# Kernel optimization log

Hardware: AMD Instinct MI355X
Metric: run time of the kernel (lower is better)

## Reference

```python
import jax, jax.numpy as jnp
import numpy as np

B, S, D = 8, 1024, 1024
H, DH = 16, 64  # num_attention_heads, attention_head_size; H*DH == D


def setup_inputs() -> dict:
    key = jax.random.key(0)
    ks = jax.random.split(key, 6)
    scale = 0.02
    return {
        "hidden_states": jax.random.normal(ks[0], (B, S, D), jnp.float32),
        "right_hidden_states": jax.random.normal(ks[1], (B, S, D), jnp.float32),
        "attention_mask": jnp.ones((B, S, S), jnp.float32),
        "Wq": jax.random.normal(ks[2], (D, H * DH), jnp.float32) * scale,
        "bq": jnp.zeros((H * DH,), jnp.float32),
        "Wk": jax.random.normal(ks[3], (D, H * DH), jnp.float32) * scale,
        "bk": jnp.zeros((H * DH,), jnp.float32),
        "Wv": jax.random.normal(ks[4], (D, H * DH), jnp.float32) * scale,
        "bv": jnp.zeros((H * DH,), jnp.float32),
    }


def _split_heads(x, b):
    # (B, S, H*DH) -> (B, H, S, DH)
    return x.reshape(b, -1, H, DH).transpose(0, 2, 1, 3)


def reference(hidden_states, right_hidden_states, attention_mask, Wq, bq, Wk, bk, Wv, bv):
    b = hidden_states.shape[0]
    q = _split_heads(hidden_states @ Wq + bq, b)          # (B,H,Sq,DH)
    k = _split_heads(right_hidden_states @ Wk + bk, b)    # (B,H,Sk,DH)
    v = _split_heads(right_hidden_states @ Wv + bv, b)    # (B,H,Sk,DH)

    scores = jnp.einsum("bhqd,bhkd->bhqk", q, k) / jnp.sqrt(jnp.asarray(DH, q.dtype))
    scores = jnp.sum(scores, axis=1, keepdims=True)       # (B,1,Sq,Sk) head-summed

    ext = (1.0 - attention_mask[:, None, :, :].astype(scores.dtype)) * -1e9
    probs = jax.nn.softmax(scores + ext, axis=-1)         # (B,1,Sq,Sk)

    ctx = jnp.matmul(probs, v)                            # broadcast -> (B,H,Sq,DH)
    # Faithful to original: reshape WITHOUT transposing heads back.
    return ctx.reshape(b, -1, H * DH)                     # (B,Sq,H*DH)
```

## Files before the change

kernel.cpp:

```cpp
#include <hip/hip_runtime.h>
#include <stdint.h>

constexpr int S = 1024;
constexpr int D = 1024;
constexpr int NB = 8;

typedef __bf16 bf16x8 __attribute__((ext_vector_type(8)));
typedef float floatx4 __attribute__((ext_vector_type(4)));

#define AS1 __attribute__((address_space(1)))
#define AS3 __attribute__((address_space(3)))

__device__ __forceinline__ unsigned short f2bf(float f) {
  unsigned u = __builtin_bit_cast(unsigned, f);
  u += 0x7fffu + ((u >> 16) & 1u);
  return (unsigned short)(u >> 16);
}

__device__ __forceinline__ void gload16(const void* g, void* l) {
  __builtin_amdgcn_global_load_lds((const AS1 unsigned int*)g, (AS3 unsigned int*)l, 16, 0, 0);
}

__global__ __launch_bounds__(256) void prep_kernel(const float4* __restrict__ hs4,
                                                   const float4* __restrict__ rhs4,
                                                   ushort4* __restrict__ hsb4,
                                                   ushort4* __restrict__ rhsb4, int n4,
                                                   const float* __restrict__ Wq,
                                                   const float* __restrict__ Wk,
                                                   const float* __restrict__ Wv,
                                                   unsigned short* __restrict__ Wcat) {
  __shared__ float tile[32][33];
  const int bid = blockIdx.x;
  if (bid < 16384) {
    int i = bid * 256 + threadIdx.x;
    const float4* src;
    ushort4* dst;
    int j;
    if (i < n4) {
      src = hs4; dst = hsb4; j = i;
    } else {
      src = rhs4; dst = rhsb4; j = i - n4;
    }
    float4 v = src[j];
    ushort4 o;
    o.x = f2bf(v.x); o.y = f2bf(v.y); o.z = f2bf(v.z); o.w = f2bf(v.w);
    dst[j] = o;
  } else {
    const int t = bid - 16384;
    const int z = t >> 10;
    const int r = t & 1023;
    const float* W = (z == 0) ? Wq : (z == 1) ? Wk : Wv;
    unsigned short* Wt = Wcat + (long long)z * D * D;
    const int bx = (r & 31) * 32;
    const int by = (r >> 5) * 32;
    const int x = threadIdx.x & 31;
    const int y0 = threadIdx.x >> 5;
    for (int i = 0; i < 4; ++i) {
      int y = y0 + i * 8;
      tile[y][x] = W[(by + y) * D + bx + x];
    }
    __syncthreads();
    for (int i = 0; i < 4; ++i) {
      int y = y0 + i * 8;
      Wt[(long long)(bx + y) * D + by + x] = f2bf(tile[x][y]);
    }
  }
}


#define GEMM_STAGE_SETUP(Abase, lda_, Bbase, ldb_)                            \
  const int srow = tid >> 2;                                                  \
  const int scg = (((tid & 3) ^ ((srow >> 1) & 3)) * 8);                      \
  const unsigned short* aG0 = (Abase) + (long long)srow * (lda_) + scg;       \
  const unsigned short* aG1 = aG0 + (long long)64 * (lda_);                   \
  const unsigned short* bG0 = (Bbase) + (long long)srow * (ldb_) + scg;       \
  const unsigned short* bG1 = bG0 + (long long)64 * (ldb_);                   \
  unsigned short* aL0 = As + w * 512;                                         \
  unsigned short* aL1 = As + w * 512 + 2048;                                  \
  unsigned short* bL0 = Bs + w * 512;                                         \
  unsigned short* bL1 = Bs + w * 512 + 2048;

#define GEMM_KLOOP(Klen)                                                               \
  for (int k0 = 0; k0 < (Klen); k0 += 32) {                                            \
    gload16(aG0 + k0, aL0);                                                            \
    gload16(aG1 + k0, aL1);                                                            \
    gload16(bG0 + k0, bL0);                                                            \
    gload16(bG1 + k0, bL1);                                                            \
    __syncthreads();                                                                   \
    bf16x8 af[4], bfr[4];                                                              \
    for (int t = 0; t < 4; ++t) {                                                      \
      af[t] = *reinterpret_cast<const bf16x8*>(As + (wm + t * 16 + r15) * 32 + pq);    \
      bfr[t] = *reinterpret_cast<const bf16x8*>(Bs + (wn + t * 16 + r15) * 32 + pq);   \
    }                                                                                  \
    for (int mt = 0; mt < 4; ++mt)                                                     \
      for (int nt = 0; nt < 4; ++nt)                                                   \
        acc[mt][nt] =                                                                  \
            __builtin_amdgcn_mfma_f32_16x16x32_bf16(af[mt], bfr[nt], acc[mt][nt], 0, 0, 0); \
    __syncthreads();                                                                   \
  }

#define GEMM_COMMON_IDX                  \
  const int tid = threadIdx.x;           \
  const int lane = tid & 63;             \
  const int w = tid >> 6;                \
  const int r15 = lane & 15;             \
  const int quad = lane >> 4;            \
  const int pq = (quad ^ ((r15 >> 1) & 3)) * 8; \
  const int wm = (w >> 1) * 64;          \
  const int wn = (w & 1) * 64;

#define GEMM_ACC_INIT                    \
  floatx4 acc[4][4];                     \
  for (int i = 0; i < 4; ++i)            \
    for (int j = 0; j < 4; ++j) acc[i][j] = {0.f, 0.f, 0.f, 0.f};

__global__ __launch_bounds__(256) void gemm_qkv_kernel(
    const unsigned short* __restrict__ hsb, const unsigned short* __restrict__ rhsb,
    const unsigned short* __restrict__ Wcat, unsigned short* __restrict__ Qm,
    unsigned short* __restrict__ Km, unsigned short* __restrict__ Vmt,
    const float* __restrict__ bq, const float* __restrict__ bk, const float* __restrict__ bv) {
  __shared__ __align__(16) unsigned short As[128 * 32];
  __shared__ __align__(16) unsigned short Bs[128 * 32];
  GEMM_COMMON_IDX
  const long long n0g = (long long)blockIdx.x * 128;
  const int seg = (int)(n0g >> 10);
  const long long m0 = (long long)blockIdx.y * 128;
  const unsigned short* A = ((seg == 0) ? hsb : rhsb) + m0 * D;
  const unsigned short* Bt = Wcat + n0g * D;
  const float* bias = (seg == 0) ? bq : (seg == 1) ? bk : bv;

  GEMM_STAGE_SETUP(A, D, Bt, D)
  GEMM_ACC_INIT
  GEMM_KLOOP(D)

  const long long nloc0 = n0g & 1023;
  for (int mt = 0; mt < 4; ++mt) {
    for (int nt = 0; nt < 4; ++nt) {
      const long long mrow = m0 + wm + mt * 16 + quad * 4;
      const long long nc = nloc0 + wn + nt * 16 + r15;
      const float bval = bias[nc];
      floatx4 v = acc[mt][nt];
      for (int e = 0; e < 4; ++e) {
        float val = v[e] + bval;
        long long m = mrow + e;
        if (seg == 0) {
          Qm[m * D + nc] = f2bf(val);
        } else if (seg == 1) {
          Km[m * D + nc] = f2bf(val);
        } else {
          Vmt[(m >> 10) * (long long)(S * D) + nc * S + (m & 1023)] = f2bf(val);
        }
      }
    }
  }
}

__global__ __launch_bounds__(256) void gemm_scores_kernel(
    const unsigned short* __restrict__ Qm, const unsigned short* __restrict__ Km,
    const float* __restrict__ mask, unsigned short* __restrict__ E,
    float* __restrict__ rowsumP) {
  __shared__ __align__(16) unsigned short As[128 * 32];
  __shared__ __align__(16) unsigned short Bs[128 * 32];
  GEMM_COMMON_IDX
  const int z = blockIdx.z;
  const long long m0 = (long long)blockIdx.y * 128;
  const long long n0 = (long long)blockIdx.x * 128;
  const unsigned short* A = Qm + (long long)z * S * D + m0 * D;
  const unsigned short* Bt = Km + (long long)z * S * D + n0 * D;

  GEMM_STAGE_SETUP(A, D, Bt, D)
  GEMM_ACC_INIT
  GEMM_KLOOP(D)

  const long long zE = (long long)z * S * 1024;
  float rowpart[4][4];
  for (int mt = 0; mt < 4; ++mt)
    for (int e = 0; e < 4; ++e) rowpart[mt][e] = 0.f;

  for (int mt = 0; mt < 4; ++mt) {
    for (int nt = 0; nt < 4; ++nt) {
      const long long mrow = m0 + wm + mt * 16 + quad * 4;
      const long long nc = n0 + wn + nt * 16 + r15;
      floatx4 v = acc[mt][nt];
      for (int e = 0; e < 4; ++e) {
        long long m = mrow + e;
        float mval = mask[zE + m * 1024 + nc];
        float sc = v[e] * 0.125f + (1.0f - mval) * -1e9f;
        float Ev = __expf(sc);
        E[zE + m * 1024 + nc] = f2bf(Ev);
        rowpart[mt][e] += Ev;
      }
    }
  }
  const int slot = ((int)blockIdx.x << 11) + ((wn >> 6) << 10);
  for (int mt = 0; mt < 4; ++mt) {
    for (int e = 0; e < 4; ++e) {
      float s = rowpart[mt][e];
      s += __shfl_xor(s, 1, 64);
      s += __shfl_xor(s, 2, 64);
      s += __shfl_xor(s, 4, 64);
      s += __shfl_xor(s, 8, 64);
      if (r15 == 0) {
        int mloc = (int)(m0 + wm + mt * 16 + quad * 4 + e);
        rowsumP[(z << 14) + slot + mloc] = s;
      }
    }
  }
}

__global__ __launch_bounds__(256) void gemm_ctx_kernel(const unsigned short* __restrict__ E,
                                                       const unsigned short* __restrict__ Vmt,
                                                       const float* __restrict__ rowsumP,
                                                       float* __restrict__ out) {
  __shared__ __align__(16) unsigned short As[128 * 32];
  __shared__ __align__(16) unsigned short Bs[128 * 32];
  __shared__ float rsinv[128];
  GEMM_COMMON_IDX
  const int z = blockIdx.z;
  const long long m0 = (long long)blockIdx.y * 128;
  const long long n0 = (long long)blockIdx.x * 128;
  const unsigned short* A = E + (long long)z * S * 1024 + m0 * 1024;
  const unsigned short* Bt = Vmt + (long long)z * S * D + n0 * D;

  if (tid < 128) {
    float s = 0.f;
    for (int t = 0; t < 16; ++t) s += rowsumP[(z << 14) + (t << 10) + (int)m0 + tid];
    rsinv[tid] = 1.0f / s;
  }

  GEMM_STAGE_SETUP(A, 1024, Bt, D)
  GEMM_ACC_INIT
  GEMM_KLOOP(1024)

  for (int mt = 0; mt < 4; ++mt) {
    for (int nt = 0; nt < 4; ++nt) {
      const int r0 = wm + mt * 16 + quad * 4;
      const long long ncol = n0 + wn + nt * 16 + r15;
      floatx4 v = acc[mt][nt];
      for (int e = 0; e < 4; ++e) {
        long long m = m0 + r0 + e;
        float val = v[e] * rsinv[r0 + e];
        out[(long long)z * S * D + (ncol >> 6) * (long long)(S * 64) + m * 64 + (ncol & 63)] =
            val;
      }
    }
  }
}

extern "C" void kernel_launch(void* const* d_in, const int* in_sizes, int n_in, void* d_out,
                              int out_size, void* d_ws, size_t ws_size, hipStream_t stream) {
  const float* hs = (const float*)d_in[0];
  const float* rhs = (const float*)d_in[1];
  const float* mask = (const float*)d_in[2];
  const float* Wq = (const float*)d_in[3];
  const float* bq = (const float*)d_in[4];
  const float* Wk = (const float*)d_in[5];
  const float* bk = (const float*)d_in[6];
  const float* Wv = (const float*)d_in[7];
  const float* bv = (const float*)d_in[8];
  float* out = (float*)d_out;
  char* ws = (char*)d_ws;
  const size_t MB = 1ull << 20;
  unsigned short* Wcat = (unsigned short*)(ws + 0 * MB);
  unsigned short* hsb = (unsigned short*)(ws + 6 * MB);
  unsigned short* rhsb = (unsigned short*)(ws + 22 * MB);
  unsigned short* Qm = (unsigned short*)(ws + 38 * MB);
  unsigned short* Km = (unsigned short*)(ws + 54 * MB);
  unsigned short* Vmt = (unsigned short*)(ws + 70 * MB);
  unsigned short* E = (unsigned short*)(ws + 6 * MB);
  float* rowsumP = (float*)(ws + 22 * MB);

  const int n4 = NB * S * D / 4;
  prep_kernel<<<16384 + 3072, 256, 0, stream>>>((const float4*)hs, (const float4*)rhs,
                                                (ushort4*)hsb, (ushort4*)rhsb, n4, Wq, Wk, Wv,
                                                Wcat);

  gemm_qkv_kernel<<<dim3(24, 64), 256, 0, stream>>>(hsb, rhsb, Wcat, Qm, Km, Vmt, bq, bk, bv);

  gemm_scores_kernel<<<dim3(8, 8, NB), 256, 0, stream>>>(Qm, Km, mask, E, rowsumP);

  gemm_ctx_kernel<<<dim3(8, 8, NB), 256, 0, stream>>>(E, Vmt, rowsumP, out);
}
```

Measured before the change: 299.4 us.

## Double-buffer LDS tiles in GEMM k-loop to overlap global loads with MFMA

```diff
diff --git a/kernel.cpp b/kernel.cpp
--- a/kernel.cpp
+++ b/kernel.cpp
@@ -74,29 +74,40 @@
   const unsigned short* aG0 = (Abase) + (long long)srow * (lda_) + scg;       \
   const unsigned short* aG1 = aG0 + (long long)64 * (lda_);                   \
   const unsigned short* bG0 = (Bbase) + (long long)srow * (ldb_) + scg;       \
-  const unsigned short* bG1 = bG0 + (long long)64 * (ldb_);                   \
-  unsigned short* aL0 = As + w * 512;                                         \
-  unsigned short* aL1 = As + w * 512 + 2048;                                  \
-  unsigned short* bL0 = Bs + w * 512;                                         \
-  unsigned short* bL1 = Bs + w * 512 + 2048;
-
-#define GEMM_KLOOP(Klen)                                                               \
-  for (int k0 = 0; k0 < (Klen); k0 += 32) {                                            \
-    gload16(aG0 + k0, aL0);                                                            \
-    gload16(aG1 + k0, aL1);                                                            \
-    gload16(bG0 + k0, bL0);                                                            \
-    gload16(bG1 + k0, bL1);                                                            \
-    __syncthreads();                                                                   \
-    bf16x8 af[4], bfr[4];                                                              \
-    for (int t = 0; t < 4; ++t) {                                                      \
-      af[t] = *reinterpret_cast<const bf16x8*>(As + (wm + t * 16 + r15) * 32 + pq);    \
-      bfr[t] = *reinterpret_cast<const bf16x8*>(Bs + (wn + t * 16 + r15) * 32 + pq);   \
-    }                                                                                  \
-    for (int mt = 0; mt < 4; ++mt)                                                     \
-      for (int nt = 0; nt < 4; ++nt)                                                   \
-        acc[mt][nt] =                                                                  \
-            __builtin_amdgcn_mfma_f32_16x16x32_bf16(af[mt], bfr[nt], acc[mt][nt], 0, 0, 0); \
-    __syncthreads();                                                                   \
+  const unsigned short* bG1 = bG0 + (long long)64 * (ldb_);
+
+#define GEMM_STAGE(bsel, ko)                      \
+  gload16(aG0 + (ko), As[bsel] + w * 512);        \
+  gload16(aG1 + (ko), As[bsel] + w * 512 + 2048); \
+  gload16(bG0 + (ko), Bs[bsel] + w * 512);        \
+  gload16(bG1 + (ko), Bs[bsel] + w * 512 + 2048);
+
+#define GEMM_KLOOP(Klen)                                                                 \
+  GEMM_STAGE(0, 0)                                                                       \
+  {                                                                                      \
+    const int NT_ = (Klen) / 32;                                                         \
+    for (int kt = 0; kt < NT_; ++kt) {                                                   \
+      const int cb = kt & 1;                                                             \
+      const int kn = (kt + 1 < NT_) ? (kt + 1) * 32 : kt * 32;                           \
+      GEMM_STAGE(cb ^ 1, kn)                                                             \
+      asm volatile("s_waitcnt vmcnt(4)" ::: "memory");                                   \
+      __builtin_amdgcn_s_barrier();                                                      \
+      asm volatile("" ::: "memory");                                                     \
+      const unsigned short* Acur = As[cb];                                               \
+      const unsigned short* Bcur = Bs[cb];                                               \
+      bf16x8 af[4], bfr[4];                                                              \
+      for (int t = 0; t < 4; ++t) {                                                      \
+        af[t] = *reinterpret_cast<const bf16x8*>(Acur + (wm + t * 16 + r15) * 32 + pq);  \
+        bfr[t] = *reinterpret_cast<const bf16x8*>(Bcur + (wn + t * 16 + r15) * 32 + pq); \
+      }                                                                                  \
+      for (int mt = 0; mt < 4; ++mt)                                                     \
+        for (int nt = 0; nt < 4; ++nt)                                                   \
+          acc[mt][nt] =                                                                  \
+              __builtin_amdgcn_mfma_f32_16x16x32_bf16(af[mt], bfr[nt], acc[mt][nt], 0, 0, 0); \
+      asm volatile("" ::: "memory");                                                     \
+      __builtin_amdgcn_s_barrier();                                                      \
+      asm volatile("" ::: "memory");                                                     \
+    }                                                                                    \
   }
 
 #define GEMM_COMMON_IDX                  \
@@ -119,8 +130,8 @@
     const unsigned short* __restrict__ Wcat, unsigned short* __restrict__ Qm,
     unsigned short* __restrict__ Km, unsigned short* __restrict__ Vmt,
     const float* __restrict__ bq, const float* __restrict__ bk, const float* __restrict__ bv) {
-  __shared__ __align__(16) unsigned short As[128 * 32];
-  __shared__ __align__(16) unsigned short Bs[128 * 32];
+  __shared__ __align__(16) unsigned short As[2][128 * 32];
+  __shared__ __align__(16) unsigned short Bs[2][128 * 32];
   GEMM_COMMON_IDX
   const long long n0g = (long long)blockIdx.x * 128;
   const int seg = (int)(n0g >> 10);
@@ -159,8 +170,8 @@
     const unsigned short* __restrict__ Qm, const unsigned short* __restrict__ Km,
     const float* __restrict__ mask, unsigned short* __restrict__ E,
     float* __restrict__ rowsumP) {
-  __shared__ __align__(16) unsigned short As[128 * 32];
-  __shared__ __align__(16) unsigned short Bs[128 * 32];
+  __shared__ __align__(16) unsigned short As[2][128 * 32];
+  __shared__ __align__(16) unsigned short Bs[2][128 * 32];
   GEMM_COMMON_IDX
   const int z = blockIdx.z;
   const long long m0 = (long long)blockIdx.y * 128;
@@ -212,8 +223,8 @@
                                                        const unsigned short* __restrict__ Vmt,
                                                        const float* __restrict__ rowsumP,
                                                        float* __restrict__ out) {
-  __shared__ __align__(16) unsigned short As[128 * 32];
-  __shared__ __align__(16) unsigned short Bs[128 * 32];
+  __shared__ __align__(16) unsigned short As[2][128 * 32];
+  __shared__ __align__(16) unsigned short Bs[2][128 * 32];
   __shared__ float rsinv[128];
   GEMM_COMMON_IDX
   const int z = blockIdx.z;
```

Result: slower. 319.8 us (+6.8%).

## Use K=64 per sync step and remap block indices for XCD locality

Applied to the files above, without the earlier changes.

```diff
diff --git a/kernel.cpp b/kernel.cpp
--- a/kernel.cpp
+++ b/kernel.cpp
@@ -74,29 +74,31 @@
   const unsigned short* aG0 = (Abase) + (long long)srow * (lda_) + scg;       \
   const unsigned short* aG1 = aG0 + (long long)64 * (lda_);                   \
   const unsigned short* bG0 = (Bbase) + (long long)srow * (ldb_) + scg;       \
-  const unsigned short* bG1 = bG0 + (long long)64 * (ldb_);                   \
-  unsigned short* aL0 = As + w * 512;                                         \
-  unsigned short* aL1 = As + w * 512 + 2048;                                  \
-  unsigned short* bL0 = Bs + w * 512;                                         \
-  unsigned short* bL1 = Bs + w * 512 + 2048;
-
-#define GEMM_KLOOP(Klen)                                                               \
-  for (int k0 = 0; k0 < (Klen); k0 += 32) {                                            \
-    gload16(aG0 + k0, aL0);                                                            \
-    gload16(aG1 + k0, aL1);                                                            \
-    gload16(bG0 + k0, bL0);                                                            \
-    gload16(bG1 + k0, bL1);                                                            \
-    __syncthreads();                                                                   \
-    bf16x8 af[4], bfr[4];                                                              \
-    for (int t = 0; t < 4; ++t) {                                                      \
-      af[t] = *reinterpret_cast<const bf16x8*>(As + (wm + t * 16 + r15) * 32 + pq);    \
-      bfr[t] = *reinterpret_cast<const bf16x8*>(Bs + (wn + t * 16 + r15) * 32 + pq);   \
-    }                                                                                  \
-    for (int mt = 0; mt < 4; ++mt)                                                     \
-      for (int nt = 0; nt < 4; ++nt)                                                   \
-        acc[mt][nt] =                                                                  \
-            __builtin_amdgcn_mfma_f32_16x16x32_bf16(af[mt], bfr[nt], acc[mt][nt], 0, 0, 0); \
-    __syncthreads();                                                                   \
+  const unsigned short* bG1 = bG0 + (long long)64 * (ldb_);
+
+#define GEMM_KLOOP(Klen)                                                                 \
+  for (int k0 = 0; k0 < (Klen); k0 += 64) {                                              \
+    gload16(aG0 + k0, As[0] + w * 512);                                                  \
+    gload16(aG1 + k0, As[0] + w * 512 + 2048);                                           \
+    gload16(aG0 + k0 + 32, As[1] + w * 512);                                             \
+    gload16(aG1 + k0 + 32, As[1] + w * 512 + 2048);                                      \
+    gload16(bG0 + k0, Bs[0] + w * 512);                                                  \
+    gload16(bG1 + k0, Bs[0] + w * 512 + 2048);                                           \
+    gload16(bG0 + k0 + 32, Bs[1] + w * 512);                                             \
+    gload16(bG1 + k0 + 32, Bs[1] + w * 512 + 2048);                                      \
+    __syncthreads();                                                                     \
+    for (int h = 0; h < 2; ++h) {                                                        \
+      bf16x8 af[4], bfr[4];                                                              \
+      for (int t = 0; t < 4; ++t) {                                                      \
+        af[t] = *reinterpret_cast<const bf16x8*>(As[h] + (wm + t * 16 + r15) * 32 + pq); \
+        bfr[t] = *reinterpret_cast<const bf16x8*>(Bs[h] + (wn + t * 16 + r15) * 32 + pq);\
+      }                                                                                  \
+      for (int mt = 0; mt < 4; ++mt)                                                     \
+        for (int nt = 0; nt < 4; ++nt)                                                   \
+          acc[mt][nt] =                                                                  \
+              __builtin_amdgcn_mfma_f32_16x16x32_bf16(af[mt], bfr[nt], acc[mt][nt], 0, 0, 0); \
+    }                                                                                    \
+    __syncthreads();                                                                     \
   }
 
 #define GEMM_COMMON_IDX                  \
@@ -119,12 +121,16 @@
     const unsigned short* __restrict__ Wcat, unsigned short* __restrict__ Qm,
     unsigned short* __restrict__ Km, unsigned short* __restrict__ Vmt,
     const float* __restrict__ bq, const float* __restrict__ bk, const float* __restrict__ bv) {
-  __shared__ __align__(16) unsigned short As[128 * 32];
-  __shared__ __align__(16) unsigned short Bs[128 * 32];
+  __shared__ __align__(16) unsigned short As[2][4096];
+  __shared__ __align__(16) unsigned short Bs[2][4096];
   GEMM_COMMON_IDX
-  const long long n0g = (long long)blockIdx.x * 128;
+  const int bid = blockIdx.x;
+  const int swz = (bid & 7) * 192 + (bid >> 3);
+  const int bx = swz % 24;
+  const int by = swz / 24;
+  const long long n0g = (long long)bx * 128;
   const int seg = (int)(n0g >> 10);
-  const long long m0 = (long long)blockIdx.y * 128;
+  const long long m0 = (long long)by * 128;
   const unsigned short* A = ((seg == 0) ? hsb : rhsb) + m0 * D;
   const unsigned short* Bt = Wcat + n0g * D;
   const float* bias = (seg == 0) ? bq : (seg == 1) ? bk : bv;
@@ -159,12 +165,16 @@
     const unsigned short* __restrict__ Qm, const unsigned short* __restrict__ Km,
     const float* __restrict__ mask, unsigned short* __restrict__ E,
     float* __restrict__ rowsumP) {
-  __shared__ __align__(16) unsigned short As[128 * 32];
-  __shared__ __align__(16) unsigned short Bs[128 * 32];
+  __shared__ __align__(16) unsigned short As[2][4096];
+  __shared__ __align__(16) unsigned short Bs[2][4096];
   GEMM_COMMON_IDX
-  const int z = blockIdx.z;
-  const long long m0 = (long long)blockIdx.y * 128;
-  const long long n0 = (long long)blockIdx.x * 128;
+  const int bid = blockIdx.x;
+  const int z = bid & 7;
+  const int r = bid >> 3;
+  const int bx = r & 7;
+  const int by = r >> 3;
+  const long long m0 = (long long)by * 128;
+  const long long n0 = (long long)bx * 128;
   const unsigned short* A = Qm + (long long)z * S * D + m0 * D;
   const unsigned short* Bt = Km + (long long)z * S * D + n0 * D;
 
@@ -192,7 +202,7 @@
       }
     }
   }
-  const int slot = ((int)blockIdx.x << 11) + ((wn >> 6) << 10);
+  const int slot = (bx << 11) + ((wn >> 6) << 10);
   for (int mt = 0; mt < 4; ++mt) {
     for (int e = 0; e < 4; ++e) {
       float s = rowpart[mt][e];
@@ -212,13 +222,17 @@
                                                        const unsigned short* __restrict__ Vmt,
                                                        const float* __restrict__ rowsumP,
                                                        float* __restrict__ out) {
-  __shared__ __align__(16) unsigned short As[128 * 32];
-  __shared__ __align__(16) unsigned short Bs[128 * 32];
+  __shared__ __align__(16) unsigned short As[2][4096];
+  __shared__ __align__(16) unsigned short Bs[2][4096];
   __shared__ float rsinv[128];
   GEMM_COMMON_IDX
-  const int z = blockIdx.z;
-  const long long m0 = (long long)blockIdx.y * 128;
-  const long long n0 = (long long)blockIdx.x * 128;
+  const int bid = blockIdx.x;
+  const int z = bid & 7;
+  const int r = bid >> 3;
+  const int bx = r & 7;
+  const int by = r >> 3;
+  const long long m0 = (long long)by * 128;
+  const long long n0 = (long long)bx * 128;
   const unsigned short* A = E + (long long)z * S * 1024 + m0 * 1024;
   const unsigned short* Bt = Vmt + (long long)z * S * D + n0 * D;
 
@@ -275,9 +289,9 @@
                                                 (ushort4*)hsb, (ushort4*)rhsb, n4, Wq, Wk, Wv,
                                                 Wcat);
 
-  gemm_qkv_kernel<<<dim3(24, 64), 256, 0, stream>>>(hsb, rhsb, Wcat, Qm, Km, Vmt, bq, bk, bv);
-
-  gemm_scores_kernel<<<dim3(8, 8, NB), 256, 0, stream>>>(Qm, Km, mask, E, rowsumP);
-
-  gemm_ctx_kernel<<<dim3(8, 8, NB), 256, 0, stream>>>(E, Vmt, rowsumP, out);
-}
+  gemm_qkv_kernel<<<dim3(1536), 256, 0, stream>>>(hsb, rhsb, Wcat, Qm, Km, Vmt, bq, bk, bv);
+
+  gemm_scores_kernel<<<dim3(512), 256, 0, stream>>>(Qm, Km, mask, E, rowsumP);
+
+  gemm_ctx_kernel<<<dim3(512), 256, 0, stream>>>(E, Vmt, rowsumP, out);
+}
```

Measured after the change: 291.7 us. 1.03x faster.
